# Performance work log

Hardware: AMD Instinct MI355X
Metric: run time of the kernel (lower is better)

## Reference

```python
import jax, jax.numpy as jnp
import numpy as np

V, T, E, H, K, L, B = 96, 16, 64, 4, 16, 4, 16384  # vocab, ctx, emb, heads, head_size, blocks, batch


def setup_inputs() -> dict:
    key = jax.random.key(0)
    ks = jax.random.split(key, 12)
    def n(k, shape, s=0.02):
        return jax.random.normal(k, shape, jnp.float32) * s
    return dict(
        data=jax.random.randint(ks[0], (B, T), 0, V),
        tok_emb=n(ks[1], (V, E)),
        pos_emb=n(ks[2], (T, E)),
        Wq=n(ks[3], (L, H, E, K)), Wk=n(ks[4], (L, H, E, K)), Wv=n(ks[5], (L, H, E, K)),
        Wo=n(ks[6], (L, E, E)), bo=jnp.zeros((L, E), jnp.float32),
        ln1_g=jnp.ones((L, E), jnp.float32), ln1_b=jnp.zeros((L, E), jnp.float32),
        ln2_g=jnp.ones((L, E), jnp.float32), ln2_b=jnp.zeros((L, E), jnp.float32),
        W1=n(ks[7], (L, E, E)), b1=jnp.zeros((L, E), jnp.float32),
        W2=n(ks[8], (L, E, E)), b2=jnp.zeros((L, E), jnp.float32),
        Wout=n(ks[9], (E, V)), bout=jnp.zeros((V,), jnp.float32),
    )


def _ln(x, g, b, eps=1e-5):
    m = x.mean(-1, keepdims=True)
    v = ((x - m) ** 2).mean(-1, keepdims=True)
    return (x - m) * jax.lax.rsqrt(v + eps) * g + b


def reference(data, tok_emb, pos_emb, Wq, Wk, Wv, Wo, bo, ln1_g, ln1_b, ln2_g, ln2_b, W1, b1, W2, b2, Wout, bout):
    # dropout is identity in eval mode
    Tcur = data.shape[1]
    x = tok_emb[data] + pos_emb[None, :Tcur]  # [B,T,E]
    scale = 1.0 / np.sqrt(K)
    for l in range(L):  # fixed small number of structurally distinct blocks
        q = jnp.einsum('bte,hek->bhtk', x, Wq[l])
        k = jnp.einsum('bte,hek->bhtk', x, Wk[l])
        v = jnp.einsum('bte,hek->bhtk', x, Wv[l])
        attn = jax.nn.softmax(jnp.einsum('bhtk,bhsk->bhts', q, k) * scale, axis=-1)
        o = jnp.einsum('bhts,bhsk->bhtk', attn, v)
        o = o.transpose(0, 2, 1, 3).reshape(x.shape[0], Tcur, E)  # concat heads
        x1 = _ln(x + o @ Wo[l] + bo[l], ln1_g[l], ln1_b[l])
        ff = jax.nn.relu(x1 @ W1[l] + b1[l]) @ W2[l] + b2[l]
        x = _ln(x1 + ff, ln2_g[l], ln2_b[l])
    return x @ Wout + bout  # [B,T,V]
```

## Files before the change

kernel.cpp:

```cpp
#include <hip/hip_runtime.h>

#define T_ 16
#define E_ 64
#define V_ 96
#define L_ 4

typedef unsigned int u32;
typedef unsigned short u16;
typedef __attribute__((ext_vector_type(8))) short bf16x8;
typedef __attribute__((ext_vector_type(4))) float f32x4;

#define MFMA(a, b, c) __builtin_amdgcn_mfma_f32_16x16x32_bf16(a, b, c, 0, 0, 0)
#define SCHED_FENCE() __builtin_amdgcn_sched_barrier(0)

#define OFF_TQ 0
#define OFF_TK 16384
#define OFF_TV 32768
#define OFF_TWO 49152
#define OFF_TW1 65536
#define OFF_TW2 81920
#define OFF_TWOUT 98304
#define PREP_TOT 104448

__device__ __forceinline__ short f2b_rne(float f) {
  u32 u = __float_as_uint(f);
  u32 r = (u + 0x7fffu + ((u >> 16) & 1u)) >> 16;
  return (short)r;
}
__device__ __forceinline__ float b2f(short s) {
  return __uint_as_float(((u32)(u16)s) << 16);
}
__device__ __forceinline__ u32 pack2_ru(float a, float b) {
  return __builtin_amdgcn_perm(__float_as_uint(a) + 0x8000u,
                               __float_as_uint(b) + 0x8000u, 0x03020706u);
}
__device__ __forceinline__ bf16x8 pk4z(f32x4 a) {
  union { bf16x8 v; u32 w[4]; } u;
  u.w[0] = pack2_ru(a[0], a[1]);
  u.w[1] = pack2_ru(a[2], a[3]);
  u.w[2] = 0u;
  u.w[3] = 0u;
  return u.v;
}

__global__ void __launch_bounds__(256) prep_weights(
    const float* __restrict__ Wq, const float* __restrict__ Wk,
    const float* __restrict__ Wv, const float* __restrict__ Wo,
    const float* __restrict__ W1, const float* __restrict__ W2,
    const float* __restrict__ Wout, short* __restrict__ wpo) {
  int id = blockIdx.x * 256 + threadIdx.x;
  if (id >= PREP_TOT) return;
  float v;
  if (id < OFF_TWO) {
    int which = id >> 14;
    int r = id & 16383;
    int l = r >> 12, n = (r >> 6) & 63, e = r & 63;
    int h = n >> 4, kq = n & 15;
    const float* W = which == 0 ? Wq : (which == 1 ? Wk : Wv);
    v = W[((l * 4 + h) * 64 + e) * 16 + kq];
  } else if (id < OFF_TWOUT) {
    int id2 = id - OFF_TWO;
    int which = id2 >> 14;
    int r = id2 & 16383;
    int l = r >> 12, n = (r >> 6) & 63, e = r & 63;
    const float* W = which == 0 ? Wo : (which == 1 ? W1 : W2);
    v = W[(l * 64 + e) * 64 + n];
  } else {
    int r = id - OFF_TWOUT;
    int n = r >> 6, e = r & 63;
    v = Wout[e * 96 + n];
  }
  wpo[id] = f2b_rne(v);
}

__device__ __forceinline__ void ln64(float vals[4][4]) {
  float sm = 0.f;
#pragma unroll
  for (int t = 0; t < 4; ++t)
#pragma unroll
    for (int r = 0; r < 4; ++r) sm += vals[t][r];
  sm += __shfl_xor(sm, 16); sm += __shfl_xor(sm, 32);
  float mean = sm * 0.015625f;
  float s2 = 0.f;
#pragma unroll
  for (int t = 0; t < 4; ++t)
#pragma unroll
    for (int r = 0; r < 4; ++r) { float d = vals[t][r] - mean; s2 = fmaf(d, d, s2); }
  s2 += __shfl_xor(s2, 16); s2 += __shfl_xor(s2, 32);
  float rst = rsqrtf(s2 * 0.015625f + 1e-5f);
#pragma unroll
  for (int t = 0; t < 4; ++t)
#pragma unroll
    for (int r = 0; r < 4; ++r) vals[t][r] = (vals[t][r] - mean) * rst;
}

__global__ void __launch_bounds__(256, 3) bert_mfma(
    const int* __restrict__ data,
    const float* __restrict__ tok_emb, const float* __restrict__ pos_emb,
    const float* __restrict__ bo, const float* __restrict__ ln1g,
    const float* __restrict__ ln1b, const float* __restrict__ ln2g,
    const float* __restrict__ ln2b, const float* __restrict__ b1,
    const float* __restrict__ b2, const float* __restrict__ bout,
    const short* __restrict__ wp, float* __restrict__ out) {
  __shared__ __align__(16) short R[4][2][16][72];

  const int w = threadIdx.x >> 6;
  const int lane = threadIdx.x & 63;
  const int m = lane & 15;
  const int qq = lane >> 4;
  const int seq0 = blockIdx.x * 8 + w * 2;

  short(*ar[2])[72] = {R[w][0], R[w][1]};

#pragma unroll
  for (int s = 0; s < 2; ++s) {
    const int t = lane >> 2;
    const int c0 = (lane & 3) * 16;
    const int tok = data[(seq0 + s) * T_ + t];
    const float4* tp = (const float4*)(tok_emb + tok * E_ + c0);
    const float4* pp = (const float4*)(pos_emb + t * E_ + c0);
    u32 buf[8];
#pragma unroll
    for (int q = 0; q < 4; ++q) {
      float4 a = tp[q], b = pp[q];
      buf[q * 2 + 0] = pack2_ru(a.x + b.x, a.y + b.y);
      buf[q * 2 + 1] = pack2_ru(a.z + b.z, a.w + b.w);
    }
    ((bf16x8*)&ar[s][t][c0])[0] = ((bf16x8*)buf)[0];
    *(bf16x8*)&ar[s][t][c0 + 8] = ((bf16x8*)(buf + 4))[0];
  }

  float xres[2][4][4];
#pragma unroll
  for (int s = 0; s < 2; ++s)
#pragma unroll
    for (int t = 0; t < 4; ++t) {
      uint2 du = *(uint2*)&ar[s][m][t * 16 + qq * 4];
      xres[s][t][0] = b2f((short)(du.x & 0xffffu));
      xres[s][t][1] = b2f((short)(du.x >> 16));
      xres[s][t][2] = b2f((short)(du.y & 0xffffu));
      xres[s][t][3] = b2f((short)(du.y >> 16));
    }

  const short s1b = (short)0x3F80;
  const bf16x8 ones8 = {s1b, s1b, s1b, s1b, s1b, s1b, s1b, s1b};
  const f32x4 z4 = {0.f, 0.f, 0.f, 0.f};

#pragma unroll 1
  for (int l = 0; l < L_; ++l) {
    const short* TQ = wp + OFF_TQ + l * 4096;
    const short* TK = wp + OFF_TK + l * 4096;
    const short* TV = wp + OFF_TV + l * 4096;
    const short* TWO = wp + OFF_TWO + l * 4096;
    const short* TW1 = wp + OFF_TW1 + l * 4096;
    const short* TW2 = wp + OFF_TW2 + l * 4096;

    bf16x8 ax0[2], ax1[2];
#pragma unroll
    for (int s = 0; s < 2; ++s) {
      ax0[s] = *(const bf16x8*)&ar[s][m][qq * 8];
      ax1[s] = *(const bf16x8*)&ar[s][m][32 + qq * 8];
    }
    SCHED_FENCE();

#pragma unroll 1
    for (int h = 0; h < 4; ++h) {
      const int bn = (h * 16 + m) * 64 + qq * 8;
      bf16x8 wq0 = *(const bf16x8*)(TQ + bn), wq1 = *(const bf16x8*)(TQ + bn + 32);
      bf16x8 wk0 = *(const bf16x8*)(TK + bn), wk1 = *(const bf16x8*)(TK + bn + 32);
      bf16x8 wv0 = *(const bf16x8*)(TV + bn), wv1 = *(const bf16x8*)(TV + bn + 32);
#pragma unroll
      for (int s = 0; s < 2; ++s) {
        f32x4 qT = MFMA(wq0, ax0[s], z4); qT = MFMA(wq1, ax1[s], qT);
        f32x4 kT = MFMA(wk0, ax0[s], z4); kT = MFMA(wk1, ax1[s], kT);
        f32x4 vv = MFMA(ax0[s], wv0, z4); vv = MFMA(ax1[s], wv1, vv);
        bf16x8 qpk = pk4z(qT), kpk = pk4z(kT), vpk = pk4z(vv);
        f32x4 sT = MFMA(kpk, qpk, z4);
        f32x4 ev;
#pragma unroll
        for (int r = 0; r < 4; ++r) ev[r] = __expf(sT[r] * 0.25f);
        bf16x8 ppk = pk4z(ev);
        f32x4 oT = MFMA(vpk, ppk, z4);
        f32x4 rs = MFMA(ones8, ppk, z4);
        float inv = __builtin_amdgcn_rcpf(rs[0]);
        *(uint2*)&ar[s][m][h * 16 + qq * 4] =
            make_uint2(pack2_ru(oT[0] * inv, oT[1] * inv),
                       pack2_ru(oT[2] * inv, oT[3] * inv));
      }
    }
    SCHED_FENCE();

    {
      bf16x8 ao0[2], ao1[2];
#pragma unroll
      for (int s = 0; s < 2; ++s) {
        ao0[s] = *(const bf16x8*)&ar[s][m][qq * 8];
        ao1[s] = *(const bf16x8*)&ar[s][m][32 + qq * 8];
      }
#pragma unroll
      for (int t = 0; t < 4; ++t) {
        const int bn = (t * 16 + m) * 64 + qq * 8;
        bf16x8 w0 = *(const bf16x8*)(TWO + bn), w1 = *(const bf16x8*)(TWO + bn + 32);
        float4 bc = *(const float4*)(bo + l * E_ + t * 16 + qq * 4);
#pragma unroll
        for (int s = 0; s < 2; ++s) {
          f32x4 d = MFMA(w0, ao0[s], z4); d = MFMA(w1, ao1[s], d);
          xres[s][t][0] += d[0] + bc.x; xres[s][t][1] += d[1] + bc.y;
          xres[s][t][2] += d[2] + bc.z; xres[s][t][3] += d[3] + bc.w;
        }
      }
#pragma unroll
      for (int s = 0; s < 2; ++s) ln64(xres[s]);
#pragma unroll
      for (int t = 0; t < 4; ++t) {
        float4 g4 = *(const float4*)(ln1g + l * E_ + t * 16 + qq * 4);
        float4 b4 = *(const float4*)(ln1b + l * E_ + t * 16 + qq * 4);
#pragma unroll
        for (int s = 0; s < 2; ++s) {
          float x0 = fmaf(xres[s][t][0], g4.x, b4.x);
          float x1v = fmaf(xres[s][t][1], g4.y, b4.y);
          float x2 = fmaf(xres[s][t][2], g4.z, b4.z);
          float x3 = fmaf(xres[s][t][3], g4.w, b4.w);
          xres[s][t][0] = x0; xres[s][t][1] = x1v;
          xres[s][t][2] = x2; xres[s][t][3] = x3;
          *(uint2*)&ar[s][m][t * 16 + qq * 4] =
              make_uint2(pack2_ru(x0, x1v), pack2_ru(x2, x3));
        }
      }
    }
    SCHED_FENCE();

    {
      bf16x8 a10[2], a11[2];
#pragma unroll
      for (int s = 0; s < 2; ++s) {
        a10[s] = *(const bf16x8*)&ar[s][m][qq * 8];
        a11[s] = *(const bf16x8*)&ar[s][m][32 + qq * 8];
      }
#pragma unroll 1
      for (int t = 0; t < 4; ++t) {
        const int bn = (t * 16 + m) * 64 + qq * 8;
        bf16x8 w0 = *(const bf16x8*)(TW1 + bn), w1 = *(const bf16x8*)(TW1 + bn + 32);
        float4 bc = *(const float4*)(b1 + l * E_ + t * 16 + qq * 4);
#pragma unroll
        for (int s = 0; s < 2; ++s) {
          f32x4 acc = MFMA(w0, a10[s], z4); acc = MFMA(w1, a11[s], acc);
          float h0 = fmaxf(acc[0] + bc.x, 0.f), h1v = fmaxf(acc[1] + bc.y, 0.f);
          float h2 = fmaxf(acc[2] + bc.z, 0.f), h3 = fmaxf(acc[3] + bc.w, 0.f);
          *(uint2*)&ar[s][m][t * 16 + qq * 4] =
              make_uint2(pack2_ru(h0, h1v), pack2_ru(h2, h3));
        }
      }
    }
    SCHED_FENCE();

    {
      bf16x8 a20[2], a21[2];
#pragma unroll
      for (int s = 0; s < 2; ++s) {
        a20[s] = *(const bf16x8*)&ar[s][m][qq * 8];
        a21[s] = *(const bf16x8*)&ar[s][m][32 + qq * 8];
      }
#pragma unroll
      for (int t = 0; t < 4; ++t) {
        const int bn = (t * 16 + m) * 64 + qq * 8;
        bf16x8 w0 = *(const bf16x8*)(TW2 + bn), w1 = *(const bf16x8*)(TW2 + bn + 32);
        float4 bc = *(const float4*)(b2 + l * E_ + t * 16 + qq * 4);
#pragma unroll
        for (int s = 0; s < 2; ++s) {
          f32x4 d = MFMA(w0, a20[s], z4); d = MFMA(w1, a21[s], d);
          xres[s][t][0] += d[0] + bc.x; xres[s][t][1] += d[1] + bc.y;
          xres[s][t][2] += d[2] + bc.z; xres[s][t][3] += d[3] + bc.w;
        }
      }
#pragma unroll
      for (int s = 0; s < 2; ++s) ln64(xres[s]);
#pragma unroll
      for (int t = 0; t < 4; ++t) {
        float4 g4 = *(const float4*)(ln2g + l * E_ + t * 16 + qq * 4);
        float4 b4 = *(const float4*)(ln2b + l * E_ + t * 16 + qq * 4);
#pragma unroll
        for (int s = 0; s < 2; ++s) {
          float x0 = fmaf(xres[s][t][0], g4.x, b4.x);
          float x1v = fmaf(xres[s][t][1], g4.y, b4.y);
          float x2 = fmaf(xres[s][t][2], g4.z, b4.z);
          float x3 = fmaf(xres[s][t][3], g4.w, b4.w);
          xres[s][t][0] = x0; xres[s][t][1] = x1v;
          xres[s][t][2] = x2; xres[s][t][3] = x3;
          *(uint2*)&ar[s][m][t * 16 + qq * 4] =
              make_uint2(pack2_ru(x0, x1v), pack2_ru(x2, x3));
        }
      }
    }
    SCHED_FENCE();
  }

  {
    bf16x8 af0[2], af1[2];
#pragma unroll
    for (int s = 0; s < 2; ++s) {
      af0[s] = *(const bf16x8*)&ar[s][m][qq * 8];
      af1[s] = *(const bf16x8*)&ar[s][m][32 + qq * 8];
    }
    const short* TWOUT = wp + OFF_TWOUT;
#pragma unroll 1
    for (int t = 0; t < 6; ++t) {
      const int bn = (t * 16 + m) * 64 + qq * 8;
      bf16x8 w0 = *(const bf16x8*)(TWOUT + bn), w1 = *(const bf16x8*)(TWOUT + bn + 32);
      float4 bc = *(const float4*)(bout + t * 16 + qq * 4);
#pragma unroll
      for (int s = 0; s < 2; ++s) {
        f32x4 acc = MFMA(w0, af0[s], z4); acc = MFMA(w1, af1[s], acc);
        float4 o4 = make_float4(acc[0] + bc.x, acc[1] + bc.y,
                                acc[2] + bc.z, acc[3] + bc.w);
        *(float4*)&out[((seq0 + s) * T_ + m) * V_ + t * 16 + qq * 4] = o4;
      }
    }
  }
}

extern "C" void kernel_launch(void* const* d_in, const int* in_sizes, int n_in,
                              void* d_out, int out_size, void* d_ws, size_t ws_size,
                              hipStream_t stream) {
  const int*   data    = (const int*)d_in[0];
  const float* tok_emb = (const float*)d_in[1];
  const float* pos_emb = (const float*)d_in[2];
  const float* Wq      = (const float*)d_in[3];
  const float* Wk      = (const float*)d_in[4];
  const float* Wv      = (const float*)d_in[5];
  const float* Wo      = (const float*)d_in[6];
  const float* bo      = (const float*)d_in[7];
  const float* ln1g    = (const float*)d_in[8];
  const float* ln1b    = (const float*)d_in[9];
  const float* ln2g    = (const float*)d_in[10];
  const float* ln2b    = (const float*)d_in[11];
  const float* W1      = (const float*)d_in[12];
  const float* b1      = (const float*)d_in[13];
  const float* W2      = (const float*)d_in[14];
  const float* b2      = (const float*)d_in[15];
  const float* Wout    = (const float*)d_in[16];
  const float* bout    = (const float*)d_in[17];
  float* out = (float*)d_out;
  short* wp = (short*)d_ws;

  prep_weights<<<(PREP_TOT + 255) / 256, 256, 0, stream>>>(
      Wq, Wk, Wv, Wo, W1, W2, Wout, wp);

  const int B = in_sizes[0] / T_;
  bert_mfma<<<B / 8, 256, 0, stream>>>(data, tok_emb, pos_emb, bo, ln1g, ln1b,
                                       ln2g, ln2b, b1, b2, bout, wp, out);
}
```

Measured before the change: 348.8 us.

## Permute weight K-dimension so MFMA outputs feed next MFMA in registers without LDS

The prep kernel now stores every weight matrix with its reduction dimension permuted (kperm) to match the per-lane element layout of MFMA accumulator outputs. The main kernel can then pack each stage's fp32 results straight into bf16x8 operand registers for the next MFMA, which removes the per-wave LDS scratch buffer and all its round-trip stores and loads. The head loop is also fully unrolled. The aim is to cut LDS traffic and latency between stages and possibly raise occupancy. In exchange, register pressure rises and correctness depends on the permutation matching the hardware fragment layout exactly.

New measurement: 484.6 us. +38.9%, slower.

```diff
diff --git a/kernel.cpp b/kernel.cpp
--- a/kernel.cpp
+++ b/kernel.cpp
@@ -22,6 +22,11 @@
 #define OFF_TWOUT 98304
 #define PREP_TOT 104448
 
+__device__ __forceinline__ int kperm(int k) {
+  int f = k >> 5, i = k & 7, qq = (k >> 3) & 3;
+  return f * 32 + (i >> 2) * 16 + qq * 4 + (i & 3);
+}
+
 __device__ __forceinline__ short f2b_rne(float f) {
   u32 u = __float_as_uint(f);
   u32 r = (u + 0x7fffu + ((u >> 16) & 1u)) >> 16;
@@ -40,6 +45,11 @@
   u.w[1] = pack2_ru(a[2], a[3]);
   u.w[2] = 0u;
   u.w[3] = 0u;
+  return u.v;
+}
+__device__ __forceinline__ bf16x8 mk8(u32 a, u32 b, u32 c, u32 d) {
+  union { bf16x8 v; u32 w[4]; } u;
+  u.w[0] = a; u.w[1] = b; u.w[2] = c; u.w[3] = d;
   return u.v;
 }
 
@@ -54,7 +64,7 @@
   if (id < OFF_TWO) {
     int which = id >> 14;
     int r = id & 16383;
-    int l = r >> 12, n = (r >> 6) & 63, e = r & 63;
+    int l = r >> 12, n = (r >> 6) & 63, e = kperm(r & 63);
     int h = n >> 4, kq = n & 15;
     const float* W = which == 0 ? Wq : (which == 1 ? Wk : Wv);
     v = W[((l * 4 + h) * 64 + e) * 16 + kq];
@@ -62,12 +72,12 @@
     int id2 = id - OFF_TWO;
     int which = id2 >> 14;
     int r = id2 & 16383;
-    int l = r >> 12, n = (r >> 6) & 63, e = r & 63;
+    int l = r >> 12, n = (r >> 6) & 63, e = kperm(r & 63);
     const float* W = which == 0 ? Wo : (which == 1 ? W1 : W2);
     v = W[(l * 64 + e) * 64 + n];
   } else {
     int r = id - OFF_TWOUT;
-    int n = r >> 6, e = r & 63;
+    int n = r >> 6, e = kperm(r & 63);
     v = Wout[e * 96 + n];
   }
   wpo[id] = f2b_rne(v);
@@ -102,49 +112,38 @@
     const float* __restrict__ ln2b, const float* __restrict__ b1,
     const float* __restrict__ b2, const float* __restrict__ bout,
     const short* __restrict__ wp, float* __restrict__ out) {
-  __shared__ __align__(16) short R[4][2][16][72];
-
   const int w = threadIdx.x >> 6;
   const int lane = threadIdx.x & 63;
   const int m = lane & 15;
   const int qq = lane >> 4;
   const int seq0 = blockIdx.x * 8 + w * 2;
 
-  short(*ar[2])[72] = {R[w][0], R[w][1]};
-
-#pragma unroll
-  for (int s = 0; s < 2; ++s) {
-    const int t = lane >> 2;
-    const int c0 = (lane & 3) * 16;
-    const int tok = data[(seq0 + s) * T_ + t];
-    const float4* tp = (const float4*)(tok_emb + tok * E_ + c0);
-    const float4* pp = (const float4*)(pos_emb + t * E_ + c0);
-    u32 buf[8];
-#pragma unroll
-    for (int q = 0; q < 4; ++q) {
-      float4 a = tp[q], b = pp[q];
-      buf[q * 2 + 0] = pack2_ru(a.x + b.x, a.y + b.y);
-      buf[q * 2 + 1] = pack2_ru(a.z + b.z, a.w + b.w);
-    }
-    ((bf16x8*)&ar[s][t][c0])[0] = ((bf16x8*)buf)[0];
-    *(bf16x8*)&ar[s][t][c0 + 8] = ((bf16x8*)(buf + 4))[0];
-  }
-
-  float xres[2][4][4];
-#pragma unroll
-  for (int s = 0; s < 2; ++s)
-#pragma unroll
-    for (int t = 0; t < 4; ++t) {
-      uint2 du = *(uint2*)&ar[s][m][t * 16 + qq * 4];
-      xres[s][t][0] = b2f((short)(du.x & 0xffffu));
-      xres[s][t][1] = b2f((short)(du.x >> 16));
-      xres[s][t][2] = b2f((short)(du.y & 0xffffu));
-      xres[s][t][3] = b2f((short)(du.y >> 16));
-    }
-
   const short s1b = (short)0x3F80;
   const bf16x8 ones8 = {s1b, s1b, s1b, s1b, s1b, s1b, s1b, s1b};
   const f32x4 z4 = {0.f, 0.f, 0.f, 0.f};
+
+  bf16x8 ax0[2], ax1[2];
+  float xres[2][4][4];
+
+#pragma unroll
+  for (int s = 0; s < 2; ++s) {
+    const int tok = data[(seq0 + s) * T_ + m];
+    u32 xw[8];
+#pragma unroll
+    for (int T = 0; T < 4; ++T) {
+      float4 te = *(const float4*)(tok_emb + tok * E_ + T * 16 + qq * 4);
+      float4 pe = *(const float4*)(pos_emb + m * E_ + T * 16 + qq * 4);
+      u32 lo = pack2_ru(te.x + pe.x, te.y + pe.y);
+      u32 hi = pack2_ru(te.z + pe.z, te.w + pe.w);
+      xw[T * 2] = lo; xw[T * 2 + 1] = hi;
+      xres[s][T][0] = b2f((short)(lo & 0xffffu));
+      xres[s][T][1] = b2f((short)(lo >> 16));
+      xres[s][T][2] = b2f((short)(hi & 0xffffu));
+      xres[s][T][3] = b2f((short)(hi >> 16));
+    }
+    ax0[s] = mk8(xw[0], xw[1], xw[2], xw[3]);
+    ax1[s] = mk8(xw[4], xw[5], xw[6], xw[7]);
+  }
 
 #pragma unroll 1
   for (int l = 0; l < L_; ++l) {
@@ -155,15 +154,8 @@
     const short* TW1 = wp + OFF_TW1 + l * 4096;
     const short* TW2 = wp + OFF_TW2 + l * 4096;
 
-    bf16x8 ax0[2], ax1[2];
-#pragma unroll
-    for (int s = 0; s < 2; ++s) {
-      ax0[s] = *(const bf16x8*)&ar[s][m][qq * 8];
-      ax1[s] = *(const bf16x8*)&ar[s][m][32 + qq * 8];
-    }
-    SCHED_FENCE();
-
-#pragma unroll 1
+    u32 ow[2][8];
+#pragma unroll
     for (int h = 0; h < 4; ++h) {
       const int bn = (h * 16 + m) * 64 + qq * 8;
       bf16x8 wq0 = *(const bf16x8*)(TQ + bn), wq1 = *(const bf16x8*)(TQ + bn + 32);
@@ -183,20 +175,19 @@
         f32x4 oT = MFMA(vpk, ppk, z4);
         f32x4 rs = MFMA(ones8, ppk, z4);
         float inv = __builtin_amdgcn_rcpf(rs[0]);
-        *(uint2*)&ar[s][m][h * 16 + qq * 4] =
-            make_uint2(pack2_ru(oT[0] * inv, oT[1] * inv),
-                       pack2_ru(oT[2] * inv, oT[3] * inv));
-      }
+        ow[s][(h >> 1) * 4 + (h & 1) * 2 + 0] = pack2_ru(oT[0] * inv, oT[1] * inv);
+        ow[s][(h >> 1) * 4 + (h & 1) * 2 + 1] = pack2_ru(oT[2] * inv, oT[3] * inv);
+      }
+    }
+    bf16x8 ao0[2], ao1[2];
+#pragma unroll
+    for (int s = 0; s < 2; ++s) {
+      ao0[s] = mk8(ow[s][0], ow[s][1], ow[s][2], ow[s][3]);
+      ao1[s] = mk8(ow[s][4], ow[s][5], ow[s][6], ow[s][7]);
     }
     SCHED_FENCE();
 
     {
-      bf16x8 ao0[2], ao1[2];
-#pragma unroll
-      for (int s = 0; s < 2; ++s) {
-        ao0[s] = *(const bf16x8*)&ar[s][m][qq * 8];
-        ao1[s] = *(const bf16x8*)&ar[s][m][32 + qq * 8];
-      }
 #pragma unroll
       for (int t = 0; t < 4; ++t) {
         const int bn = (t * 16 + m) * 64 + qq * 8;
@@ -211,6 +202,7 @@
       }
 #pragma unroll
       for (int s = 0; s < 2; ++s) ln64(xres[s]);
+      u32 xw[2][8];
 #pragma unroll
       for (int t = 0; t < 4; ++t) {
         float4 g4 = *(const float4*)(ln1g + l * E_ + t * 16 + qq * 4);
@@ -223,44 +215,44 @@
           float x3 = fmaf(xres[s][t][3], g4.w, b4.w);
           xres[s][t][0] = x0; xres[s][t][1] = x1v;
           xres[s][t][2] = x2; xres[s][t][3] = x3;
-          *(uint2*)&ar[s][m][t * 16 + qq * 4] =
-              make_uint2(pack2_ru(x0, x1v), pack2_ru(x2, x3));
-        }
+          xw[s][t * 2] = pack2_ru(x0, x1v);
+          xw[s][t * 2 + 1] = pack2_ru(x2, x3);
+        }
+      }
+#pragma unroll
+      for (int s = 0; s < 2; ++s) {
+        ax0[s] = mk8(xw[s][0], xw[s][1], xw[s][2], xw[s][3]);
+        ax1[s] = mk8(xw[s][4], xw[s][5], xw[s][6], xw[s][7]);
       }
     }
     SCHED_FENCE();
 
+    bf16x8 ah0[2], ah1[2];
     {
-      bf16x8 a10[2], a11[2];
-#pragma unroll
-      for (int s = 0; s < 2; ++s) {
-        a10[s] = *(const bf16x8*)&ar[s][m][qq * 8];
-        a11[s] = *(const bf16x8*)&ar[s][m][32 + qq * 8];
-      }
-#pragma unroll 1
+      u32 hw[2][8];
+#pragma unroll
       for (int t = 0; t < 4; ++t) {
         const int bn = (t * 16 + m) * 64 + qq * 8;
         bf16x8 w0 = *(const bf16x8*)(TW1 + bn), w1 = *(const bf16x8*)(TW1 + bn + 32);
         float4 bc = *(const float4*)(b1 + l * E_ + t * 16 + qq * 4);
 #pragma unroll
         for (int s = 0; s < 2; ++s) {
-          f32x4 acc = MFMA(w0, a10[s], z4); acc = MFMA(w1, a11[s], acc);
+          f32x4 acc = MFMA(w0, ax0[s], z4); acc = MFMA(w1, ax1[s], acc);
           float h0 = fmaxf(acc[0] + bc.x, 0.f), h1v = fmaxf(acc[1] + bc.y, 0.f);
           float h2 = fmaxf(acc[2] + bc.z, 0.f), h3 = fmaxf(acc[3] + bc.w, 0.f);
-          *(uint2*)&ar[s][m][t * 16 + qq * 4] =
-              make_uint2(pack2_ru(h0, h1v), pack2_ru(h2, h3));
-        }
+          hw[s][t * 2] = pack2_ru(h0, h1v);
+          hw[s][t * 2 + 1] = pack2_ru(h2, h3);
+        }
+      }
+#pragma unroll
+      for (int s = 0; s < 2; ++s) {
+        ah0[s] = mk8(hw[s][0], hw[s][1], hw[s][2], hw[s][3]);
+        ah1[s] = mk8(hw[s][4], hw[s][5], hw[s][6], hw[s][7]);
       }
     }
     SCHED_FENCE();
 
     {
-      bf16x8 a20[2], a21[2];
-#pragma unroll
-      for (int s = 0; s < 2; ++s) {
-        a20[s] = *(const bf16x8*)&ar[s][m][qq * 8];
-        a21[s] = *(const bf16x8*)&ar[s][m][32 + qq * 8];
-      }
 #pragma unroll
       for (int t = 0; t < 4; ++t) {
         const int bn = (t * 16 + m) * 64 + qq * 8;
@@ -268,13 +260,14 @@
         float4 bc = *(const float4*)(b2 + l * E_ + t * 16 + qq * 4);
 #pragma unroll
         for (int s = 0; s < 2; ++s) {
-          f32x4 d = MFMA(w0, a20[s], z4); d = MFMA(w1, a21[s], d);
+          f32x4 d = MFMA(w0, ah0[s], z4); d = MFMA(w1, ah1[s], d);
           xres[s][t][0] += d[0] + bc.x; xres[s][t][1] += d[1] + bc.y;
           xres[s][t][2] += d[2] + bc.z; xres[s][t][3] += d[3] + bc.w;
         }
       }
 #pragma unroll
       for (int s = 0; s < 2; ++s) ln64(xres[s]);
+      u32 xw[2][8];
 #pragma unroll
       for (int t = 0; t < 4; ++t) {
         float4 g4 = *(const float4*)(ln2g + l * E_ + t * 16 + qq * 4);
@@ -287,21 +280,20 @@
           float x3 = fmaf(xres[s][t][3], g4.w, b4.w);
           xres[s][t][0] = x0; xres[s][t][1] = x1v;
           xres[s][t][2] = x2; xres[s][t][3] = x3;
-          *(uint2*)&ar[s][m][t * 16 + qq * 4] =
-              make_uint2(pack2_ru(x0, x1v), pack2_ru(x2, x3));
-        }
+          xw[s][t * 2] = pack2_ru(x0, x1v);
+          xw[s][t * 2 + 1] = pack2_ru(x2, x3);
+        }
+      }
+#pragma unroll
+      for (int s = 0; s < 2; ++s) {
+        ax0[s] = mk8(xw[s][0], xw[s][1], xw[s][2], xw[s][3]);
+        ax1[s] = mk8(xw[s][4], xw[s][5], xw[s][6], xw[s][7]);
       }
     }
     SCHED_FENCE();
   }
 
   {
-    bf16x8 af0[2], af1[2];
-#pragma unroll
-    for (int s = 0; s < 2; ++s) {
-      af0[s] = *(const bf16x8*)&ar[s][m][qq * 8];
-      af1[s] = *(const bf16x8*)&ar[s][m][32 + qq * 8];
-    }
     const short* TWOUT = wp + OFF_TWOUT;
 #pragma unroll 1
     for (int t = 0; t < 6; ++t) {
@@ -310,7 +302,7 @@
       float4 bc = *(const float4*)(bout + t * 16 + qq * 4);
 #pragma unroll
       for (int s = 0; s < 2; ++s) {
-        f32x4 acc = MFMA(w0, af0[s], z4); acc = MFMA(w1, af1[s], acc);
+        f32x4 acc = MFMA(w0, ax0[s], z4); acc = MFMA(w1, ax1[s], acc);
         float4 o4 = make_float4(acc[0] + bc.x, acc[1] + bc.y,
                                 acc[2] + bc.z, acc[3] + bc.w);
         *(float4*)&out[((seq0 + s) * T_ + m) * V_ + t * 16 + qq * 4] = o4;
```
